# Kernel tuning notes

Hardware: AMD Instinct MI355X
Metric: run time of the kernel (lower is better)

## Reference

```python
import jax, jax.numpy as jnp
import numpy as np

N_PTS = 262144
N_GAUSS = 2048
NZ, NY, NX = 100, 100, 100
MAX_SCALE = 0.02
BG = -1.0
CUTOFF = 9.0  # 3-sigma Mahalanobis cutoff
CHUNK = 1024


def quat_to_rot(q):
    # q: [G,4] normalized quaternion (r, x, y, z) as in 3DGS
    r, x, y, z = q[:, 0], q[:, 1], q[:, 2], q[:, 3]
    R = jnp.stack([
        1 - 2 * (y * y + z * z), 2 * (x * y - r * z), 2 * (x * z + r * y),
        2 * (x * y + r * z), 1 - 2 * (x * x + z * z), 2 * (y * z - r * x),
        2 * (x * z - r * y), 2 * (y * z + r * x), 1 - 2 * (x * x + y * y),
    ], axis=-1)
    return R.reshape(-1, 3, 3)


def setup_inputs() -> dict:
    key = jax.random.key(0)
    k = jax.random.split(key, 7)
    x = jax.random.uniform(k[0], (N_PTS, 3), jnp.float32, -1.0, 1.0)
    xyz = jax.random.uniform(k[1], (N_GAUSS, 3), jnp.float32)
    # raw log-scales so exp(raw) ~ 0.01 (Gaussians a few cells wide)
    scaling_raw = jax.random.normal(k[2], (N_GAUSS, 3), jnp.float32) * 0.3 + jnp.log(0.01)
    rotation_raw = jax.random.normal(k[3], (N_GAUSS, 4), jnp.float32)
    weight_raw = jax.random.normal(k[4], (N_GAUSS, 1), jnp.float32)
    values_raw = jax.random.normal(k[5], (N_GAUSS, 1), jnp.float32)
    valid_grid = jax.random.uniform(k[6], (NZ * NY * NX,)) < 0.8
    return {"x": x, "xyz": xyz, "scaling_raw": scaling_raw,
            "rotation_raw": rotation_raw, "weight_raw": weight_raw,
            "values_raw": values_raw, "valid_grid": valid_grid}


def _forward(x, xyz, scaling_raw, rotation_raw, weight_raw, values_raw, valid_grid):
    # valid-mask lookup from nearest grid cell
    x01 = (x + 1.0) * 0.5
    ix = jnp.clip(jnp.round(x01[:, 0] * (NX - 1)).astype(jnp.int32), 0, NX - 1)
    iy = jnp.clip(jnp.round(x01[:, 1] * (NY - 1)).astype(jnp.int32), 0, NY - 1)
    iz = jnp.clip(jnp.round(x01[:, 2] * (NZ - 1)).astype(jnp.int32), 0, NZ - 1)
    flat_idx = iz * (NY * NX) + iy * NX + ix
    valid = valid_grid[flat_idx]
    # world coords: mesh normalized to [0,1]^3 so vol_min=0, extent=1
    xw = x01
    # activations on Gaussian parameters
    s = jnp.exp(scaling_raw)
    r = jnp.linalg.norm(s, axis=1, keepdims=True) + 1e-8
    r_soft = MAX_SCALE * jnp.tanh(r / MAX_SCALE)
    s = s * (r_soft / r)                           # capped scales [G,3]
    qn = rotation_raw / jnp.maximum(
        jnp.linalg.norm(rotation_raw, axis=1, keepdims=True), 1e-12)
    R = quat_to_rot(qn)                            # [G,3,3]
    inv_s2 = 1.0 / (s * s)
    A = jnp.einsum('gik,gk,gjk->gij', R, inv_s2, R)  # inverse covariance [G,3,3]
    w = jax.nn.sigmoid(weight_raw[:, 0])           # [G]
    v = jax.nn.sigmoid(values_raw[:, 0])           # [G]
    wv = w * v
    xs = xw.reshape(-1, CHUNK, 3)                  # scan over point chunks

    def step(_, xc):
        d = xc[:, None, :] - xyz[None, :, :]       # [C,G,3]
        qd = jnp.einsum('cgi,gij,cgj->cg', d, A, d)
        g = jnp.where(qd <= CUTOFF, jnp.exp(-0.5 * qd), 0.0)  # [C,G]
        den = g @ w
        num = g @ wv
        y = jnp.where(den > 0, num / jnp.where(den > 0, den, 1.0), BG)
        return None, y

    _, ys = jax.lax.scan(step, None, xs)
    y = jnp.where(valid, ys.reshape(-1), 0.0)
    return y.reshape(-1, 1)


def reference(x, xyz, scaling_raw, rotation_raw, weight_raw, values_raw, valid_grid):
    return _forward(x, xyz, scaling_raw, rotation_raw, weight_raw, values_raw, valid_grid)
```

## Files before the change

kernel.cpp:

```cpp
#include <hip/hip_runtime.h>
#include <hip/hip_bf16.h>

namespace {

constexpr int GRIDC = 16;
constexpr int NCELL = GRIDC * GRIDC * GRIDC;
constexpr int CAP   = 48;

__device__ __forceinline__ float sigmoid_(float v) {
    if (v >= 0.0f) { float e = expf(-v); return 1.0f / (1.0f + e); }
    float e = expf(v); return e / (1.0f + e);
}

__global__ void __launch_bounds__(1024)
VEG_setup(const unsigned char* __restrict__ vg,
          const float* __restrict__ xyz, const float* __restrict__ sraw,
          const float* __restrict__ rraw, const float* __restrict__ wraw,
          const float* __restrict__ vraw,
          float* __restrict__ gdata, int* __restrict__ counts,
          int* __restrict__ lists, int* __restrict__ mode_p, int ng) {
    __shared__ int scount[NCELL];
    __shared__ int f1, f3;
    if (threadIdx.x == 0) { f1 = 0; f3 = 0; }
    for (int c = threadIdx.x; c < NCELL; c += 1024) scount[c] = 0;
    __syncthreads();

    int l1 = 0, l3 = 0;
    for (int i = threadIdx.x; i < 4096; i += 1024) {
        unsigned char b = vg[i];
        if (b) {
            int m = i & 3;
            if (m == 1) l1 = 1;
            if (m == 3) l3 = 1;
        }
    }
    if (l1) atomicOr(&f1, 1);
    if (l3) atomicOr(&f3, 1);

    for (int g = threadIdx.x; g < ng; g += 1024) {
        float s0 = expf(sraw[g * 3 + 0]);
        float s1 = expf(sraw[g * 3 + 1]);
        float s2 = expf(sraw[g * 3 + 2]);
        float r  = sqrtf(s0 * s0 + s1 * s1 + s2 * s2) + 1e-8f;
        float rs = 0.02f * tanhf(r / 0.02f);
        float fsc = rs / r;
        s0 *= fsc; s1 *= fsc; s2 *= fsc;

        float q0 = rraw[g * 4 + 0], q1 = rraw[g * 4 + 1];
        float q2 = rraw[g * 4 + 2], q3 = rraw[g * 4 + 3];
        float qn = fmaxf(sqrtf(q0 * q0 + q1 * q1 + q2 * q2 + q3 * q3), 1e-12f);
        float inv = 1.0f / qn;
        float rr = q0 * inv, qx = q1 * inv, qy = q2 * inv, qz = q3 * inv;
        float R00 = 1.0f - 2.0f * (qy * qy + qz * qz);
        float R01 = 2.0f * (qx * qy - rr * qz);
        float R02 = 2.0f * (qx * qz + rr * qy);
        float R10 = 2.0f * (qx * qy + rr * qz);
        float R11 = 1.0f - 2.0f * (qx * qx + qz * qz);
        float R12 = 2.0f * (qy * qz - rr * qx);
        float R20 = 2.0f * (qx * qz - rr * qy);
        float R21 = 2.0f * (qy * qz + rr * qx);
        float R22 = 1.0f - 2.0f * (qx * qx + qy * qy);

        float i0 = 1.0f / (s0 * s0), i1 = 1.0f / (s1 * s1), i2 = 1.0f / (s2 * s2);
        float a00 = R00 * R00 * i0 + R01 * R01 * i1 + R02 * R02 * i2;
        float a11 = R10 * R10 * i0 + R11 * R11 * i1 + R12 * R12 * i2;
        float a22 = R20 * R20 * i0 + R21 * R21 * i1 + R22 * R22 * i2;
        float a01 = R00 * R10 * i0 + R01 * R11 * i1 + R02 * R12 * i2;
        float a02 = R00 * R20 * i0 + R01 * R21 * i1 + R02 * R22 * i2;
        float a12 = R10 * R20 * i0 + R11 * R21 * i1 + R12 * R22 * i2;

        float w  = sigmoid_(wraw[g]);
        float v  = sigmoid_(vraw[g]);

        float cx = xyz[g * 3 + 0], cy = xyz[g * 3 + 1], cz = xyz[g * 3 + 2];
        float rad = 3.0f * fmaxf(fmaxf(s0, s1), s2);
        rad = rad * 1.001f + 1e-6f;

        float* o = gdata + (size_t)g * 12;
        o[0] = cx;  o[1] = cy;  o[2] = cz;  o[3] = a00;
        o[4] = a11; o[5] = a22; o[6] = a01; o[7] = a02;
        o[8] = a12; o[9] = w;   o[10] = w * v; o[11] = rad;

        int xlo = max(0, (int)floorf((cx - rad) * (float)GRIDC));
        int xhi = min(GRIDC - 1, (int)floorf((cx + rad) * (float)GRIDC));
        int ylo = max(0, (int)floorf((cy - rad) * (float)GRIDC));
        int yhi = min(GRIDC - 1, (int)floorf((cy + rad) * (float)GRIDC));
        int zlo = max(0, (int)floorf((cz - rad) * (float)GRIDC));
        int zhi = min(GRIDC - 1, (int)floorf((cz + rad) * (float)GRIDC));
        for (int zz = zlo; zz <= zhi; ++zz)
            for (int yy = ylo; yy <= yhi; ++yy)
                for (int xx = xlo; xx <= xhi; ++xx) {
                    int cell = (zz * GRIDC + yy) * GRIDC + xx;
                    int slot = atomicAdd(&scount[cell], 1);
                    if (slot < CAP) lists[cell * CAP + slot] = g;
                }
    }
    __syncthreads();
    for (int c = threadIdx.x; c < NCELL; c += 1024) counts[c] = scount[c];
    if (threadIdx.x == 0) *mode_p = f1 ? 0 : (f3 ? 2 : 1);
}

__global__ void __launch_bounds__(256)
VEG_splat(const float* __restrict__ x, const float* __restrict__ gdata,
          const int* __restrict__ counts, const int* __restrict__ lists,
          const void* __restrict__ valid, const int* __restrict__ mode_p,
          float* __restrict__ out, int npts) {
    __shared__ float shx[768];
    int base = blockIdx.x * 256;
    int nrem = npts - base;
    if (nrem >= 256) {
        if (threadIdx.x < 192)
            ((float4*)shx)[threadIdx.x] = ((const float4*)(x + (size_t)base * 3))[threadIdx.x];
    } else {
        for (int j = threadIdx.x; j < nrem * 3; j += 256)
            shx[j] = x[(size_t)base * 3 + j];
    }
    __syncthreads();

    int i = base + threadIdx.x;
    if (i >= npts) return;

    float px = (shx[threadIdx.x * 3 + 0] + 1.0f) * 0.5f;
    float py = (shx[threadIdx.x * 3 + 1] + 1.0f) * 0.5f;
    float pz = (shx[threadIdx.x * 3 + 2] + 1.0f) * 0.5f;

    int ix = min(99, max(0, (int)rintf(px * 99.0f)));
    int iy = min(99, max(0, (int)rintf(py * 99.0f)));
    int iz = min(99, max(0, (int)rintf(pz * 99.0f)));
    int flat = iz * 10000 + iy * 100 + ix;

    int mode = *mode_p;
    bool vb;
    if (mode == 0)      vb = ((const unsigned char*)valid)[flat] != 0;
    else if (mode == 1) vb = ((const int*)valid)[flat] != 0;
    else                vb = ((const float*)valid)[flat] != 0.0f;

    int cx = min(GRIDC - 1, (int)(px * (float)GRIDC));
    int cy = min(GRIDC - 1, (int)(py * (float)GRIDC));
    int cz = min(GRIDC - 1, (int)(pz * (float)GRIDC));
    int cell = (cz * GRIDC + cy) * GRIDC + cx;

    int cnt = min(counts[cell], CAP);
    const int* lst = lists + cell * CAP;

    float den = 0.0f, num = 0.0f;
    for (int j = 0; j < cnt; ++j) {
        int g = lst[j];
        const float4* gd = (const float4*)(gdata + (size_t)g * 12);
        float4 A = gd[0], B = gd[1], C = gd[2];
        float dx = px - A.x, dy = py - A.y, dz = pz - A.z;
        float qd = A.w * dx * dx + B.x * dy * dy + B.y * dz * dz +
                   2.0f * (B.z * dx * dy + B.w * dx * dz + C.x * dy * dz);
        if (qd <= 9.0f) {
            float e = expf(-0.5f * qd);
            den = fmaf(C.y, e, den);
            num = fmaf(C.z, e, num);
        }
    }
    float y = (den > 0.0f) ? (num / den) : -1.0f;
    out[i] = vb ? y : 0.0f;
}

__global__ void VEG_detect(const unsigned char* vg, int* mode) {
    __shared__ int f1, f3;
    if (threadIdx.x == 0) { f1 = 0; f3 = 0; }
    __syncthreads();
    for (int i = threadIdx.x; i < 4096; i += blockDim.x) {
        unsigned char b = vg[i];
        if (b) {
            int m = i & 3;
            if (m == 1) atomicOr(&f1, 1);
            if (m == 3) atomicOr(&f3, 1);
        }
    }
    __syncthreads();
    if (threadIdx.x == 0) *mode = f1 ? 0 : (f3 ? 2 : 1);
}

__global__ void __launch_bounds__(256)
VEG_brute(const float* __restrict__ x, const float* __restrict__ xyz,
          const float* __restrict__ sraw, const float* __restrict__ rraw,
          const float* __restrict__ wraw, const float* __restrict__ vraw,
          const void* __restrict__ valid, const int* __restrict__ mode_p,
          float* __restrict__ out, int npts, int ng) {
    __shared__ float sh[256 * 12];
    int i = blockIdx.x * blockDim.x + threadIdx.x;
    bool inb = i < npts;
    float px = 0, py = 0, pz = 0; int flat = 0;
    if (inb) {
        px = (x[i * 3 + 0] + 1.0f) * 0.5f;
        py = (x[i * 3 + 1] + 1.0f) * 0.5f;
        pz = (x[i * 3 + 2] + 1.0f) * 0.5f;
        int ix = min(99, max(0, (int)rintf(px * 99.0f)));
        int iy = min(99, max(0, (int)rintf(py * 99.0f)));
        int iz = min(99, max(0, (int)rintf(pz * 99.0f)));
        flat = iz * 10000 + iy * 100 + ix;
    }
    float den = 0.0f, num = 0.0f;
    for (int base = 0; base < ng; base += 256) {
        __syncthreads();
        int g = base + threadIdx.x;
        if (g < ng) {
            float s0 = expf(sraw[g * 3 + 0]);
            float s1 = expf(sraw[g * 3 + 1]);
            float s2 = expf(sraw[g * 3 + 2]);
            float r  = sqrtf(s0 * s0 + s1 * s1 + s2 * s2) + 1e-8f;
            float rs = 0.02f * tanhf(r / 0.02f);
            float fsc = rs / r;
            s0 *= fsc; s1 *= fsc; s2 *= fsc;
            float q0 = rraw[g * 4 + 0], q1 = rraw[g * 4 + 1];
            float q2 = rraw[g * 4 + 2], q3 = rraw[g * 4 + 3];
            float qn = fmaxf(sqrtf(q0 * q0 + q1 * q1 + q2 * q2 + q3 * q3), 1e-12f);
            float inv = 1.0f / qn;
            float rr = q0 * inv, qx = q1 * inv, qy = q2 * inv, qz = q3 * inv;
            float R00 = 1.0f - 2.0f * (qy * qy + qz * qz);
            float R01 = 2.0f * (qx * qy - rr * qz);
            float R02 = 2.0f * (qx * qz + rr * qy);
            float R10 = 2.0f * (qx * qy + rr * qz);
            float R11 = 1.0f - 2.0f * (qx * qx + qz * qz);
            float R12 = 2.0f * (qy * qz - rr * qx);
            float R20 = 2.0f * (qx * qz - rr * qy);
            float R21 = 2.0f * (qy * qz + rr * qx);
            float R22 = 1.0f - 2.0f * (qx * qx + qy * qy);
            float i0 = 1.0f / (s0 * s0), i1 = 1.0f / (s1 * s1), i2 = 1.0f / (s2 * s2);
            float* o = sh + threadIdx.x * 12;
            o[0] = xyz[g * 3 + 0]; o[1] = xyz[g * 3 + 1]; o[2] = xyz[g * 3 + 2];
            o[3] = R00 * R00 * i0 + R01 * R01 * i1 + R02 * R02 * i2;
            o[4] = R10 * R10 * i0 + R11 * R11 * i1 + R12 * R12 * i2;
            o[5] = R20 * R20 * i0 + R21 * R21 * i1 + R22 * R22 * i2;
            o[6] = R00 * R10 * i0 + R01 * R11 * i1 + R02 * R12 * i2;
            o[7] = R00 * R20 * i0 + R01 * R21 * i1 + R02 * R22 * i2;
            o[8] = R10 * R20 * i0 + R11 * R21 * i1 + R12 * R22 * i2;
            float w = sigmoid_(wraw[g]);
            float v = sigmoid_(vraw[g]);
            o[9] = w; o[10] = w * v; o[11] = 0.0f;
        }
        __syncthreads();
        int tile = min(256, ng - base);
        if (inb) {
            for (int j = 0; j < tile; ++j) {
                const float* o = sh + j * 12;
                float dx = px - o[0], dy = py - o[1], dz = pz - o[2];
                float qd = o[3] * dx * dx + o[4] * dy * dy + o[5] * dz * dz +
                           2.0f * (o[6] * dx * dy + o[7] * dx * dz + o[8] * dy * dz);
                if (qd <= 9.0f) {
                    float e = expf(-0.5f * qd);
                    den = fmaf(o[9], e, den);
                    num = fmaf(o[10], e, num);
                }
            }
        }
    }
    if (inb) {
        int mode = *mode_p;
        bool vb;
        if (mode == 0)      vb = ((const unsigned char*)valid)[flat] != 0;
        else if (mode == 1) vb = ((const int*)valid)[flat] != 0;
        else                vb = ((const float*)valid)[flat] != 0.0f;
        float y = (den > 0.0f) ? (num / den) : -1.0f;
        out[i] = vb ? y : 0.0f;
    }
}

}

extern "C" void kernel_launch(void* const* d_in, const int* in_sizes, int n_in,
                              void* d_out, int out_size, void* d_ws, size_t ws_size,
                              hipStream_t stream) {
    const float* x    = (const float*)d_in[0];
    const float* xyz  = (const float*)d_in[1];
    const float* sraw = (const float*)d_in[2];
    const float* rraw = (const float*)d_in[3];
    const float* wraw = (const float*)d_in[4];
    const float* vraw = (const float*)d_in[5];
    const void*  valid = d_in[6];
    float* out = (float*)d_out;

    int npts = in_sizes[0] / 3;
    int ng   = in_sizes[4];

    char* ws = (char*)d_ws;
    size_t mode_off   = 0;
    size_t gdata_off  = 256;
    size_t counts_off = gdata_off + (size_t)ng * 12 * sizeof(float);
    counts_off = (counts_off + 255) & ~(size_t)255;
    size_t lists_off  = counts_off + (size_t)NCELL * sizeof(int);
    size_t total      = lists_off + (size_t)NCELL * CAP * sizeof(int);

    int* mode = (int*)(ws + mode_off);

    if (ws_size >= total) {
        float* gdata = (float*)(ws + gdata_off);
        int* counts  = (int*)(ws + counts_off);
        int* lists   = (int*)(ws + lists_off);
        VEG_setup<<<1, 1024, 0, stream>>>((const unsigned char*)valid, xyz, sraw,
                                          rraw, wraw, vraw, gdata, counts, lists,
                                          mode, ng);
        VEG_splat<<<(npts + 255) / 256, 256, 0, stream>>>(x, gdata, counts, lists,
                                                          valid, mode, out, npts);
    } else {
        VEG_detect<<<1, 256, 0, stream>>>((const unsigned char*)valid, mode);
        VEG_brute<<<(npts + 255) / 256, 256, 0, stream>>>(x, xyz, sraw, rraw, wraw,
                                                          vraw, valid, mode, out,
                                                          npts, ng);
    }
}
```

Baseline: 104.8 us.

## Store full Gaussian records per grid cell instead of index lists

The setup kernel now writes the 12-float Gaussian parameter record, padded to 16 floats, straight into each cell's bin slot, replacing the index it stored before. The splat loop then reads contiguous records with no dependent index-then-gather load. The loop also uses the fast __expf intrinsic and is unrolled by two, and the cell lookup is moved earlier so its load overlaps the valid-mask read. The cost is a much larger workspace (4096*48*64 bytes) and more global writes in the single-block setup kernel, plus a small loss of exp precision.

```diff
diff --git a/kernel.cpp b/kernel.cpp
--- a/kernel.cpp
+++ b/kernel.cpp
@@ -6,6 +6,7 @@
 constexpr int GRIDC = 16;
 constexpr int NCELL = GRIDC * GRIDC * GRIDC;
 constexpr int CAP   = 48;
+constexpr int RECF  = 16;
 
 __device__ __forceinline__ float sigmoid_(float v) {
     if (v >= 0.0f) { float e = expf(-v); return 1.0f / (1.0f + e); }
@@ -17,8 +18,8 @@
           const float* __restrict__ xyz, const float* __restrict__ sraw,
           const float* __restrict__ rraw, const float* __restrict__ wraw,
           const float* __restrict__ vraw,
-          float* __restrict__ gdata, int* __restrict__ counts,
-          int* __restrict__ lists, int* __restrict__ mode_p, int ng) {
+          float* __restrict__ recs, int* __restrict__ counts,
+          int* __restrict__ mode_p, int ng) {
     __shared__ int scount[NCELL];
     __shared__ int f1, f3;
     if (threadIdx.x == 0) { f1 = 0; f3 = 0; }
@@ -62,24 +63,20 @@
         float R22 = 1.0f - 2.0f * (qx * qx + qy * qy);
 
         float i0 = 1.0f / (s0 * s0), i1 = 1.0f / (s1 * s1), i2 = 1.0f / (s2 * s2);
-        float a00 = R00 * R00 * i0 + R01 * R01 * i1 + R02 * R02 * i2;
-        float a11 = R10 * R10 * i0 + R11 * R11 * i1 + R12 * R12 * i2;
-        float a22 = R20 * R20 * i0 + R21 * R21 * i1 + R22 * R22 * i2;
-        float a01 = R00 * R10 * i0 + R01 * R11 * i1 + R02 * R12 * i2;
-        float a02 = R00 * R20 * i0 + R01 * R21 * i1 + R02 * R22 * i2;
-        float a12 = R10 * R20 * i0 + R11 * R21 * i1 + R12 * R22 * i2;
-
-        float w  = sigmoid_(wraw[g]);
-        float v  = sigmoid_(vraw[g]);
-
-        float cx = xyz[g * 3 + 0], cy = xyz[g * 3 + 1], cz = xyz[g * 3 + 2];
+        float4 rA = make_float4(xyz[g * 3 + 0], xyz[g * 3 + 1], xyz[g * 3 + 2],
+                                R00 * R00 * i0 + R01 * R01 * i1 + R02 * R02 * i2);
+        float4 rB = make_float4(R10 * R10 * i0 + R11 * R11 * i1 + R12 * R12 * i2,
+                                R20 * R20 * i0 + R21 * R21 * i1 + R22 * R22 * i2,
+                                R00 * R10 * i0 + R01 * R11 * i1 + R02 * R12 * i2,
+                                R00 * R20 * i0 + R01 * R21 * i1 + R02 * R22 * i2);
+        float w = sigmoid_(wraw[g]);
+        float v = sigmoid_(vraw[g]);
+        float4 rC = make_float4(R10 * R20 * i0 + R11 * R21 * i1 + R12 * R22 * i2,
+                                w, w * v, 0.0f);
+
         float rad = 3.0f * fmaxf(fmaxf(s0, s1), s2);
         rad = rad * 1.001f + 1e-6f;
-
-        float* o = gdata + (size_t)g * 12;
-        o[0] = cx;  o[1] = cy;  o[2] = cz;  o[3] = a00;
-        o[4] = a11; o[5] = a22; o[6] = a01; o[7] = a02;
-        o[8] = a12; o[9] = w;   o[10] = w * v; o[11] = rad;
+        float cx = rA.x, cy = rA.y, cz = rA.z;
 
         int xlo = max(0, (int)floorf((cx - rad) * (float)GRIDC));
         int xhi = min(GRIDC - 1, (int)floorf((cx + rad) * (float)GRIDC));
@@ -92,7 +89,10 @@
                 for (int xx = xlo; xx <= xhi; ++xx) {
                     int cell = (zz * GRIDC + yy) * GRIDC + xx;
                     int slot = atomicAdd(&scount[cell], 1);
-                    if (slot < CAP) lists[cell * CAP + slot] = g;
+                    if (slot < CAP) {
+                        float4* o = (float4*)(recs + ((size_t)cell * CAP + slot) * RECF);
+                        o[0] = rA; o[1] = rB; o[2] = rC;
+                    }
                 }
     }
     __syncthreads();
@@ -101,8 +101,8 @@
 }
 
 __global__ void __launch_bounds__(256)
-VEG_splat(const float* __restrict__ x, const float* __restrict__ gdata,
-          const int* __restrict__ counts, const int* __restrict__ lists,
+VEG_splat(const float* __restrict__ x, const float* __restrict__ recs,
+          const int* __restrict__ counts,
           const void* __restrict__ valid, const int* __restrict__ mode_p,
           float* __restrict__ out, int npts) {
     __shared__ float shx[768];
@@ -124,6 +124,13 @@
     float py = (shx[threadIdx.x * 3 + 1] + 1.0f) * 0.5f;
     float pz = (shx[threadIdx.x * 3 + 2] + 1.0f) * 0.5f;
 
+    int cx = min(GRIDC - 1, (int)(px * (float)GRIDC));
+    int cy = min(GRIDC - 1, (int)(py * (float)GRIDC));
+    int cz = min(GRIDC - 1, (int)(pz * (float)GRIDC));
+    int cell = (cz * GRIDC + cy) * GRIDC + cx;
+    int cnt = counts[cell];
+    const float4* rec = (const float4*)(recs + (size_t)cell * CAP * RECF);
+
     int ix = min(99, max(0, (int)rintf(px * 99.0f)));
     int iy = min(99, max(0, (int)rintf(py * 99.0f)));
     int iz = min(99, max(0, (int)rintf(pz * 99.0f)));
@@ -135,24 +142,16 @@
     else if (mode == 1) vb = ((const int*)valid)[flat] != 0;
     else                vb = ((const float*)valid)[flat] != 0.0f;
 
-    int cx = min(GRIDC - 1, (int)(px * (float)GRIDC));
-    int cy = min(GRIDC - 1, (int)(py * (float)GRIDC));
-    int cz = min(GRIDC - 1, (int)(pz * (float)GRIDC));
-    int cell = (cz * GRIDC + cy) * GRIDC + cx;
-
-    int cnt = min(counts[cell], CAP);
-    const int* lst = lists + cell * CAP;
-
+    cnt = min(cnt, CAP);
     float den = 0.0f, num = 0.0f;
+#pragma unroll 2
     for (int j = 0; j < cnt; ++j) {
-        int g = lst[j];
-        const float4* gd = (const float4*)(gdata + (size_t)g * 12);
-        float4 A = gd[0], B = gd[1], C = gd[2];
+        float4 A = rec[j * 4 + 0], B = rec[j * 4 + 1], C = rec[j * 4 + 2];
         float dx = px - A.x, dy = py - A.y, dz = pz - A.z;
         float qd = A.w * dx * dx + B.x * dy * dy + B.y * dz * dz +
                    2.0f * (B.z * dx * dy + B.w * dx * dz + C.x * dy * dz);
         if (qd <= 9.0f) {
-            float e = expf(-0.5f * qd);
+            float e = __expf(-0.5f * qd);
             den = fmaf(C.y, e, den);
             num = fmaf(C.z, e, num);
         }
@@ -281,22 +280,19 @@
 
     char* ws = (char*)d_ws;
     size_t mode_off   = 0;
-    size_t gdata_off  = 256;
-    size_t counts_off = gdata_off + (size_t)ng * 12 * sizeof(float);
-    counts_off = (counts_off + 255) & ~(size_t)255;
-    size_t lists_off  = counts_off + (size_t)NCELL * sizeof(int);
-    size_t total      = lists_off + (size_t)NCELL * CAP * sizeof(int);
+    size_t counts_off = 256;
+    size_t recs_off   = counts_off + (size_t)NCELL * sizeof(int);
+    recs_off = (recs_off + 255) & ~(size_t)255;
+    size_t total = recs_off + (size_t)NCELL * CAP * RECF * sizeof(float);
 
     int* mode = (int*)(ws + mode_off);
 
     if (ws_size >= total) {
-        float* gdata = (float*)(ws + gdata_off);
-        int* counts  = (int*)(ws + counts_off);
-        int* lists   = (int*)(ws + lists_off);
+        int*   counts = (int*)(ws + counts_off);
+        float* recs   = (float*)(ws + recs_off);
         VEG_setup<<<1, 1024, 0, stream>>>((const unsigned char*)valid, xyz, sraw,
-                                          rraw, wraw, vraw, gdata, counts, lists,
-                                          mode, ng);
-        VEG_splat<<<(npts + 255) / 256, 256, 0, stream>>>(x, gdata, counts, lists,
+                                          rraw, wraw, vraw, recs, counts, mode, ng);
+        VEG_splat<<<(npts + 255) / 256, 256, 0, stream>>>(x, recs, counts,
                                                           valid, mode, out, npts);
     } else {
         VEG_detect<<<1, 256, 0, stream>>>((const unsigned char*)valid, mode);
```

Result: slower. 133.6 us (+27.5%).
